# Optimization experiments

Hardware: AMD Instinct MI355X
Metric: run time of the kernel (lower is better)

The kernel has to match this reference:

```python
import jax, jax.numpy as jnp
import numpy as np

EMBED_DIM = 1024
NUM_HEADS = 16
HEAD_DIM = EMBED_DIM // NUM_HEADS
TGT_LEN = 1024
SRC_LEN = 1024
BSZ = 4


def setup_inputs() -> dict:
    key = jax.random.key(0)
    ks = jax.random.split(key, 7)
    query = jax.random.normal(ks[0], (TGT_LEN, BSZ, EMBED_DIM), dtype=jnp.float32)
    key_t = jax.random.normal(ks[1], (SRC_LEN, BSZ, EMBED_DIM), dtype=jnp.float32)
    # hard 0/1 multiplicative mask applied post-softmax
    hard_attention = jax.random.randint(ks[2], (BSZ, TGT_LEN, SRC_LEN), 0, 2).astype(jnp.float32)
    # xavier_uniform_ on [3E, E]
    limit = float(np.sqrt(6.0 / (3 * EMBED_DIM + EMBED_DIM)))
    in_proj_weight = jax.random.uniform(ks[3], (3 * EMBED_DIM, EMBED_DIM), dtype=jnp.float32,
                                        minval=-limit, maxval=limit)
    in_proj_bias = jnp.zeros((3 * EMBED_DIM,), dtype=jnp.float32)
    limit_o = float(np.sqrt(1.0 / EMBED_DIM))
    out_proj_weight = jax.random.uniform(ks[4], (EMBED_DIM, EMBED_DIM), dtype=jnp.float32,
                                         minval=-limit_o, maxval=limit_o)
    out_proj_bias = jnp.zeros((EMBED_DIM,), dtype=jnp.float32)
    return {
        "query": query,
        "key": key_t,
        "hard_attention": hard_attention,
        "in_proj_weight": in_proj_weight,
        "in_proj_bias": in_proj_bias,
        "out_proj_weight": out_proj_weight,
        "out_proj_bias": out_proj_bias,
    }


def reference(query, key, hard_attention, in_proj_weight, in_proj_bias,
              out_proj_weight, out_proj_bias):
    tgt_len, bsz, embed_dim = query.shape
    src_len = key.shape[0]
    h, hd = NUM_HEADS, embed_dim // NUM_HEADS
    scaling = float(hd) ** -0.5

    # QKV projections (F.linear uses y = x @ W.T + b)
    wq = in_proj_weight[:embed_dim]
    wkv = in_proj_weight[embed_dim:]
    bq = in_proj_bias[:embed_dim]
    bkv = in_proj_bias[embed_dim:]
    q = jnp.einsum('tbe,fe->tbf', query, wq) + bq          # [T,B,E]
    kv = jnp.einsum('sbe,fe->sbf', key, wkv) + bkv          # [S,B,2E]
    k, v = jnp.split(kv, 2, axis=-1)

    q = (q * scaling).reshape(tgt_len, bsz, h, hd).transpose(1, 2, 0, 3)  # [B,H,T,D]
    k = k.reshape(src_len, bsz, h, hd).transpose(1, 2, 0, 3)              # [B,H,S,D]
    v = v.reshape(src_len, bsz, h, hd).transpose(1, 2, 0, 3)              # [B,H,S,D]

    scores = jnp.einsum('bhtd,bhsd->bhts', q, k)            # [B,H,T,S]
    attn = jax.nn.softmax(scores, axis=-1)
    # dropout_p = 0.0 -> identity
    attn = attn * hard_attention[:, None, :, :]             # post-softmax hard mask

    out = jnp.einsum('bhts,bhsd->bhtd', attn, v)            # [B,H,T,D]
    out = out.transpose(2, 0, 1, 3).reshape(tgt_len, bsz, embed_dim)
    out = jnp.einsum('tbe,fe->tbf', out, out_proj_weight) + out_proj_bias

    avg_weights = attn.sum(axis=1) / h                      # [B,T,S]
    return (out, avg_weights)
```

## Files before the change

kernel.cpp:

```cpp
#include <hip/hip_runtime.h>
#include <cstdint>
#include <cstddef>

typedef __bf16 bf16x8 __attribute__((ext_vector_type(8)));
typedef float  f32x4  __attribute__((ext_vector_type(4)));
typedef unsigned short u16x8 __attribute__((ext_vector_type(8)));

__device__ __forceinline__ uint16_t f2bf(float f) {
  uint32_t u = __float_as_uint(f);
  u += 0x7fffu + ((u >> 16) & 1u);
  return (uint16_t)(u >> 16);
}
__device__ __forceinline__ float bf2f(uint16_t u) {
  return __uint_as_float((uint32_t)u << 16);
}
__device__ __forceinline__ uint32_t cvtpk(float lo, float hi) {
  uint32_t r;
  asm("v_cvt_pk_bf16_f32 %0, %1, %2" : "=v"(r) : "v"(lo), "v"(hi));
  return r;
}

__device__ __forceinline__ f32x4 mfma16(bf16x8 a, bf16x8 b, f32x4 c) {
  return __builtin_amdgcn_mfma_f32_16x16x32_bf16(a, b, c, 0, 0, 0);
}

#define GLD_TO_LDS16(gptr, lptr)                                                   \
  __builtin_amdgcn_global_load_lds(                                                \
      (const __attribute__((address_space(1))) void*)(gptr),                       \
      (__attribute__((address_space(3))) void*)(lptr), 16, 0, 0)

__global__ void prep(const float* __restrict__ q, const float* __restrict__ k,
                     const float* __restrict__ w, const float* __restrict__ wo,
                     const float* __restrict__ hard,
                     uint16_t* __restrict__ Xq, uint16_t* __restrict__ Xk,
                     uint16_t* __restrict__ Wb, uint16_t* __restrict__ Wob,
                     uint32_t* __restrict__ bits) {
  const int bid = blockIdx.x;
  if (bid < 12288) {
    int i = bid * 256 + threadIdx.x;
    const float* src;
    uint16_t* dst;
    int off;
    if (i < 1048576)      { src = q;  dst = Xq;  off = i; }
    else if (i < 2097152) { src = k;  dst = Xk;  off = i - 1048576; }
    else if (i < 2883584) { src = w;  dst = Wb;  off = i - 2097152; }
    else                  { src = wo; dst = Wob; off = i - 2883584; }
    float4 v = ((const float4*)src)[off];
    ushort4 o;
    o.x = f2bf(v.x); o.y = f2bf(v.y); o.z = f2bf(v.z); o.w = f2bf(v.w);
    ((ushort4*)dst)[off] = o;
  } else {
    int base = (bid - 12288) * 1024;
#pragma unroll
    for (int c = 0; c < 4; c++) {
      int i = base + c * 256 + threadIdx.x;
      unsigned long long m = __ballot(hard[i] != 0.0f);
      if ((threadIdx.x & 63) == 0) {
        int wd = i >> 5;
        bits[wd]     = (uint32_t)m;
        bits[wd + 1] = (uint32_t)(m >> 32);
      }
    }
  }
}

__global__ __launch_bounds__(256)
void gemm_qkv(const uint16_t* __restrict__ Xq, const uint16_t* __restrict__ Xk,
              const uint16_t* __restrict__ Wb, const float* __restrict__ ipb,
              uint16_t* __restrict__ Qb, uint16_t* __restrict__ Kb,
              uint16_t* __restrict__ Vt) {
  __shared__ __align__(16) char As[128 * 128];
  __shared__ __align__(16) char Bs[128 * 128];
  const int tid  = threadIdx.x;
  const int wave = tid >> 6, lane = tid & 63;
  const int quad = lane >> 4, l16 = lane & 15;
  const int sw = (l16 & 7) << 4;

  const int swz = (blockIdx.x & 7) * 96 + (blockIdx.x >> 3);
  const uint16_t *A, *B;
  const float* bias;
  int bm, bn, mode;
  if (swz < 256) {
    mode = 0; A = Xq; B = Wb; bias = ipb;
    bm = swz >> 3; bn = swz & 7;
  } else {
    mode = 1; A = Xk; B = Wb + (1 << 20); bias = ipb + 1024;
    int t = swz - 256; bm = t >> 4; bn = t & 15;
  }
  const int wm = (wave >> 1) << 6, wn = (wave & 1) << 6;

  const int lrow = lane >> 3;
  const int scol = ((lane & 7) ^ lrow) << 4;
  const char* Ag = (const char*)A + (size_t)(bm * 128) * 2048;
  const char* Bg = (const char*)B + (size_t)(bn * 128) * 2048;

  f32x4 acc[4][4] = {};

  for (int k0 = 0; k0 < 2048; k0 += 128) {
    __syncthreads();
#pragma unroll
    for (int j = 0; j < 4; j++) {
      const int rbase = j * 32 + wave * 8;
      GLD_TO_LDS16(Ag + (size_t)(rbase + lrow) * 2048 + k0 + scol,
                   As + rbase * 128);
      GLD_TO_LDS16(Bg + (size_t)(rbase + lrow) * 2048 + k0 + scol,
                   Bs + rbase * 128);
    }
    __syncthreads();

    bf16x8 af[4][2], bfr[4][2];
#pragma unroll
    for (int i = 0; i < 4; i++) {
      const char* pa = As + (wm + i * 16 + l16) * 128;
      const char* pb = Bs + (wn + i * 16 + l16) * 128;
#pragma unroll
      for (int ks = 0; ks < 2; ks++) {
        af[i][ks]  = *(const bf16x8*)(pa + ((ks * 64 + quad * 16) ^ sw));
        bfr[i][ks] = *(const bf16x8*)(pb + ((ks * 64 + quad * 16) ^ sw));
      }
    }
#pragma unroll
    for (int ks = 0; ks < 2; ks++)
#pragma unroll
      for (int mi = 0; mi < 4; mi++)
#pragma unroll
        for (int ni = 0; ni < 4; ni++)
          acc[mi][ni] = mfma16(af[mi][ks], bfr[ni][ks], acc[mi][ni]);
  }

#pragma unroll
  for (int mi = 0; mi < 4; mi++)
#pragma unroll
    for (int ni = 0; ni < 4; ni++)
#pragma unroll
      for (int r = 0; r < 4; r++) {
        int gi = bm * 128 + wm + mi * 16 + quad * 4 + r;
        int gf = bn * 128 + wn + ni * 16 + l16;
        float c = acc[mi][ni][r] + bias[gf];
        if (mode == 0) {
          c *= 0.125f;
          int t = gi >> 2, b = gi & 3, h = gf >> 6, d = gf & 63;
          Qb[((((size_t)b * 16 + h) * 1024 + t) << 6) + d] = f2bf(c);
        } else {
          int s = gi >> 2, b = gi & 3;
          if (gf < 1024) {
            int h = gf >> 6, d = gf & 63;
            Kb[((((size_t)b * 16 + h) * 1024 + s) << 6) + d] = f2bf(c);
          } else {
            int fv = gf - 1024, h = fv >> 6, d = fv & 63;
            Vt[((((size_t)b * 16 + h) * 64 + d) << 10) + s] = f2bf(c);
          }
        }
      }
}

__global__ __launch_bounds__(256, 2)
void attn_kernel(const uint16_t* __restrict__ qb, const uint16_t* __restrict__ kb,
                 const uint16_t* __restrict__ vtb, const uint32_t* __restrict__ bits,
                 uint16_t* __restrict__ attn_out, float* __restrict__ rlout) {
  __shared__ __align__(16) uint16_t Ks[128 * 64];
  __shared__ __align__(16) uint16_t Vs[64 * 128];
  __shared__ __align__(16) uint16_t Pb[4 * 32 * 128];

  const int bid = blockIdx.x;
  const int xcd = bid & 7, j = bid >> 3;
  const int slab = xcd * 8 + (j >> 3);
  const int b = slab >> 4, h = slab & 15;
  const int t0 = (j & 7) << 7;
  const int tid = threadIdx.x, wave = tid >> 6, lane = tid & 63;
  const int quad = lane >> 4, l16 = lane & 15;
  const int sw = (l16 & 7) << 4;
  const size_t bh = (size_t)b * 16 + h;
  const int tw = t0 + wave * 32;
  const int ta = tw + l16, tb = ta + 16;
  char* PwA = (char*)(Pb + wave * (32 * 128)) + l16 * 256;
  char* PwB = PwA + 16 * 256;

  const uint16_t* qA = qb + ((bh << 10) + ta) * 64;
  bf16x8 aqA0 = *(const bf16x8*)(qA + quad * 8);
  bf16x8 aqA1 = *(const bf16x8*)(qA + 32 + quad * 8);
  bf16x8 aqB0 = *(const bf16x8*)(qA + 1024 + quad * 8);
  bf16x8 aqB1 = *(const bf16x8*)(qA + 1024 + 32 + quad * 8);

  f32x4 accA[4] = {}, accB[4] = {};
  float smA = 0.f, smB = 0.f;

  const int kr = tid >> 3, kc8 = tid & 7;
  const int vr = tid >> 4, vc16 = tid & 15;

  const uint32_t* bA = bits + (((size_t)(b << 10) + ta) << 5);
  const uint32_t* bB = bits + (((size_t)(b << 10) + tb) << 5);

  u16x8 kreg[4], vreg[4];
#pragma unroll
  for (int r = 0; r < 4; r++)
    kreg[r] = *(const u16x8*)(kb + (bh << 16) + (size_t)(r * 256 + tid) * 8);
#pragma unroll
  for (int r = 0; r < 4; r++)
    vreg[r] = *(const u16x8*)(vtb + (((bh << 6) + r * 16 + vr) << 10) + vc16 * 8);
  uint4 uA = *(const uint4*)bA;
  uint4 uB = *(const uint4*)bB;

  for (int sc = 0; sc < 8; sc++) {
    uint32_t wA[4] = {uA.x >> (quad * 4), uA.y >> (quad * 4),
                      uA.z >> (quad * 4), uA.w >> (quad * 4)};
    uint32_t wB[4] = {uB.x >> (quad * 4), uB.y >> (quad * 4),
                      uB.z >> (quad * 4), uB.w >> (quad * 4)};

    __syncthreads();
#pragma unroll
    for (int r = 0; r < 4; r++) {
      const int row = r * 32 + kr;
      *(u16x8*)((char*)Ks + row * 128 + ((kc8 * 16) ^ ((row & 7) << 4))) = kreg[r];
    }
#pragma unroll
    for (int r = 0; r < 4; r++) {
      const int row = r * 16 + vr;
      *(u16x8*)((char*)Vs + row * 256 + ((vc16 * 16) ^ ((row & 7) << 4))) = vreg[r];
    }
    __syncthreads();

    if (sc < 7) {
      const uint16_t* kbase = kb + (bh << 16) + (size_t)(sc + 1) * 8192;
#pragma unroll
      for (int r = 0; r < 4; r++)
        kreg[r] = *(const u16x8*)(kbase + (size_t)(r * 256 + tid) * 8);
#pragma unroll
      for (int r = 0; r < 4; r++)
        vreg[r] = *(const u16x8*)(vtb + (((bh << 6) + r * 16 + vr) << 10) +
                                  (sc + 1) * 128 + vc16 * 8);
      uA = *(const uint4*)(bA + (sc + 1) * 4);
      uB = *(const uint4*)(bB + (sc + 1) * 4);
    }

#pragma unroll
    for (int nn = 0; nn < 8; nn++) {
      const char* kbp = (const char*)Ks + (nn * 16 + l16) * 128;
      bf16x8 bk0 = *(const bf16x8*)(kbp + ((quad * 16) ^ sw));
      bf16x8 bk1 = *(const bf16x8*)(kbp + ((64 + quad * 16) ^ sw));
      f32x4 cA = {}, cB = {};
      cA = mfma16(bk0, aqA0, cA); cA = mfma16(bk1, aqA1, cA);
      cB = mfma16(bk0, aqB0, cB); cB = mfma16(bk1, aqB1, cB);
      const uint32_t mA = wA[nn >> 1] >> ((nn & 1) * 16);
      const uint32_t mB = wB[nn >> 1] >> ((nn & 1) * 16);
      float eA[4], eB[4];
#pragma unroll
      for (int r = 0; r < 4; r++) {
        eA[r] = __expf(cA[r]); smA += eA[r];
        eB[r] = __expf(cB[r]); smB += eB[r];
        eA[r] = ((mA >> r) & 1) ? eA[r] : 0.f;
        eB[r] = ((mB >> r) & 1) ? eB[r] : 0.f;
      }
      const int pc = (nn * 32 + quad * 8) ^ sw;
      *(uint2*)(PwA + pc) = make_uint2(cvtpk(eA[0], eA[1]), cvtpk(eA[2], eA[3]));
      *(uint2*)(PwB + pc) = make_uint2(cvtpk(eB[0], eB[1]), cvtpk(eB[2], eB[3]));
    }

#pragma unroll
    for (int kc = 0; kc < 4; kc++) {
      const int pcb = (kc * 64 + quad * 16) ^ sw;
      bf16x8 apA = *(const bf16x8*)(PwA + pcb);
      bf16x8 apB = *(const bf16x8*)(PwB + pcb);
#pragma unroll
      for (int dt = 0; dt < 4; dt++) {
        bf16x8 bv = *(const bf16x8*)((const char*)Vs + (dt * 16 + l16) * 256 +
                                     ((kc * 64 + quad * 16) ^ sw));
        accA[dt] = mfma16(bv, apA, accA[dt]);
        accB[dt] = mfma16(bv, apB, accB[dt]);
      }
    }
  }

  smA += __shfl_xor(smA, 16); smA += __shfl_xor(smA, 32);
  smB += __shfl_xor(smB, 16); smB += __shfl_xor(smB, 32);
  const float rlA = 1.0f / smA, rlB = 1.0f / smB;
  if (quad == 0) rlout[(bh << 10) + ta] = rlA;
  if (quad == 1) rlout[(bh << 10) + tb] = rlB;

#pragma unroll
  for (int dt = 0; dt < 4; dt++) {
    uint2 oA = make_uint2(cvtpk(accA[dt][0] * rlA, accA[dt][1] * rlA),
                          cvtpk(accA[dt][2] * rlA, accA[dt][3] * rlA));
    *(uint2*)(attn_out + ((size_t)(ta * 4 + b) << 10) + h * 64 + dt * 16 + quad * 4) = oA;
    uint2 oB = make_uint2(cvtpk(accB[dt][0] * rlB, accB[dt][1] * rlB),
                          cvtpk(accB[dt][2] * rlB, accB[dt][3] * rlB));
    *(uint2*)(attn_out + ((size_t)(tb * 4 + b) << 10) + h * 64 + dt * 16 + quad * 4) = oB;
  }
}

__global__ __launch_bounds__(256, 4)
void tail(const uint16_t* __restrict__ qb, const uint16_t* __restrict__ kb,
          const float* __restrict__ rlin, const float* __restrict__ hard,
          const uint16_t* __restrict__ Ao, const uint16_t* __restrict__ Bw,
          const float* __restrict__ opb,
          float* __restrict__ out, float* __restrict__ avgout) {
  __shared__ __align__(16) char smem[24576];
  const int bid = blockIdx.x;
  const int tid = threadIdx.x, wave = tid >> 6, lane = tid & 63;
  const int quad = lane >> 4, l16 = lane & 15;

  if (bid < 512) {
    uint16_t* Ks = (uint16_t*)smem;
    const int xcd = bid & 7, j = bid >> 3;
    const int slab = xcd * 4 + (j >> 4);
    const int b  = slab >> 3;
    const int s0 = (slab & 7) << 7;
    const int t0 = (j & 15) << 6;
    const int sw = (l16 & 7) << 4;
    const int tr = t0 + wave * 16 + l16;
    const int kr = tid >> 3, kc8 = tid & 7;

    float av[8][4] = {};

    u16x8 kreg[4];
    {
      const uint16_t* kb0 = kb + ((((size_t)b * 16) << 10) + s0) * 64;
#pragma unroll
      for (int r = 0; r < 4; r++)
        kreg[r] = *(const u16x8*)(kb0 + (size_t)(r * 256 + tid) * 8);
    }

    for (int hh = 0; hh < 16; hh++) {
      __syncthreads();
#pragma unroll
      for (int r = 0; r < 4; r++) {
        const int row = r * 32 + kr;
        *(u16x8*)((char*)Ks + row * 128 + ((kc8 * 16) ^ ((row & 7) << 4))) = kreg[r];
      }
      __syncthreads();
      if (hh < 15) {
        const uint16_t* kb2 = kb + ((((size_t)b * 16 + hh + 1) << 10) + s0) * 64;
#pragma unroll
        for (int r = 0; r < 4; r++)
          kreg[r] = *(const u16x8*)(kb2 + (size_t)(r * 256 + tid) * 8);
      }

      const size_t bh = (size_t)b * 16 + hh;
      const uint16_t* qrow = qb + ((bh << 10) + tr) * 64;
      bf16x8 aq0 = *(const bf16x8*)(qrow + quad * 8);
      bf16x8 aq1 = *(const bf16x8*)(qrow + 32 + quad * 8);
      const float rl = rlin[(bh << 10) + tr];

#pragma unroll
      for (int n = 0; n < 8; n++) {
        const char* kbp = (const char*)Ks + (n * 16 + l16) * 128;
        bf16x8 bk0 = *(const bf16x8*)(kbp + ((quad * 16) ^ sw));
        bf16x8 bk1 = *(const bf16x8*)(kbp + ((64 + quad * 16) ^ sw));
        f32x4 c = {};
        c = mfma16(bk0, aq0, c);
        c = mfma16(bk1, aq1, c);
#pragma unroll
        for (int r = 0; r < 4; r++) av[n][r] += __expf(c[r]) * rl;
      }
    }

    const float* hrow = hard + (((size_t)(b << 10) + tr) << 10) + s0 + quad * 4;
    float* orow = avgout + ((size_t)(b << 10) + tr) * 1024 + s0 + quad * 4;
#pragma unroll
    for (int n = 0; n < 8; n++) {
      float4 hm = *(const float4*)(hrow + n * 16);
      float4 f;
      f.x = av[n][0] * (hm.x != 0.f ? 0.0625f : 0.f);
      f.y = av[n][1] * (hm.y != 0.f ? 0.0625f : 0.f);
      f.z = av[n][2] * (hm.z != 0.f ? 0.0625f : 0.f);
      f.w = av[n][3] * (hm.w != 0.f ? 0.0625f : 0.f);
      *(float4*)(orow + n * 16) = f;
    }
  } else {
    char* As = smem;
    char* Bs = smem + 8192;
    const int u = bid - 512;
    const int swz = (u & 7) * 64 + (u >> 3);
    const int bm = swz >> 3, bn = swz & 7;
    const int wm = (wave >> 1) << 5, wn = (wave & 1) << 6;
    const int sw = (l16 & 7) << 4;
    const int lrow = lane >> 3;
    const int scol = ((lane & 7) ^ lrow) << 4;
    const char* Ag = (const char*)Ao + (size_t)(bm * 64) * 2048;
    const char* Bg = (const char*)Bw + (size_t)(bn * 128) * 2048;

    f32x4 acc[2][4] = {};

    for (int k0 = 0; k0 < 2048; k0 += 128) {
      __syncthreads();
#pragma unroll
      for (int jj = 0; jj < 2; jj++) {
        const int rbase = jj * 32 + wave * 8;
        GLD_TO_LDS16(Ag + (size_t)(rbase + lrow) * 2048 + k0 + scol,
                     As + rbase * 128);
      }
#pragma unroll
      for (int jj = 0; jj < 4; jj++) {
        const int rbase = jj * 32 + wave * 8;
        GLD_TO_LDS16(Bg + (size_t)(rbase + lrow) * 2048 + k0 + scol,
                     Bs + rbase * 128);
      }
      __syncthreads();

      bf16x8 af[2][2], bfr[4][2];
#pragma unroll
      for (int i = 0; i < 2; i++) {
        const char* pa = As + (wm + i * 16 + l16) * 128;
#pragma unroll
        for (int ks = 0; ks < 2; ks++)
          af[i][ks] = *(const bf16x8*)(pa + ((ks * 64 + quad * 16) ^ sw));
      }
#pragma unroll
      for (int i = 0; i < 4; i++) {
        const char* pb = Bs + (wn + i * 16 + l16) * 128;
#pragma unroll
        for (int ks = 0; ks < 2; ks++)
          bfr[i][ks] = *(const bf16x8*)(pb + ((ks * 64 + quad * 16) ^ sw));
      }
#pragma unroll
      for (int ks = 0; ks < 2; ks++)
#pragma unroll
        for (int mi = 0; mi < 2; mi++)
#pragma unroll
          for (int ni = 0; ni < 4; ni++)
            acc[mi][ni] = mfma16(af[mi][ks], bfr[ni][ks], acc[mi][ni]);
    }

#pragma unroll
    for (int mi = 0; mi < 2; mi++)
#pragma unroll
      for (int ni = 0; ni < 4; ni++)
#pragma unroll
        for (int r = 0; r < 4; r++) {
          int gi = bm * 64 + wm + mi * 16 + quad * 4 + r;
          int gf = bn * 128 + wn + ni * 16 + l16;
          out[(size_t)gi * 1024 + gf] = acc[mi][ni][r] + opb[gf];
        }
  }
}

extern "C" void kernel_launch(void* const* d_in, const int* in_sizes, int n_in,
                              void* d_out, int out_size, void* d_ws, size_t ws_size,
                              hipStream_t stream) {
  const float* query = (const float*)d_in[0];
  const float* key   = (const float*)d_in[1];
  const float* hard  = (const float*)d_in[2];
  const float* ipw   = (const float*)d_in[3];
  const float* ipb   = (const float*)d_in[4];
  const float* opw   = (const float*)d_in[5];
  const float* opb   = (const float*)d_in[6];

  char* ws = (char*)d_ws;
  const size_t MB = 1ull << 20;
  uint16_t* Xq  = (uint16_t*)(ws + 0);
  uint16_t* Xk  = (uint16_t*)(ws + 8 * MB);
  uint16_t* Wb  = (uint16_t*)(ws + 16 * MB);
  uint16_t* Wob = (uint16_t*)(ws + 22 * MB);
  uint16_t* Qb  = (uint16_t*)(ws + 24 * MB);
  uint16_t* Kb  = (uint16_t*)(ws + 32 * MB);
  uint16_t* Vt  = (uint16_t*)(ws + 40 * MB);
  uint16_t* AO  = Xq;
  float*    rlws = (float*)(ws + 8 * MB);

  float* out = (float*)d_out;
  float* avg = out + 4194304;
  uint32_t* bits = (uint32_t*)out;

  prep<<<16384, 256, 0, stream>>>(query, key, ipw, opw, hard,
                                  Xq, Xk, Wb, Wob, bits);

  gemm_qkv<<<768, 256, 0, stream>>>(Xq, Xk, Wb, ipb, Qb, Kb, Vt);

  attn_kernel<<<512, 256, 0, stream>>>(Qb, Kb, Vt, bits, AO, rlws);

  tail<<<1024, 256, 0, stream>>>(Qb, Kb, rlws, hard, AO, Wob, opb, out, avg);
}
```

Baseline: 228.8 us.

## Load V fragments directly from global and process two heads per tail iteration

The attention kernel drops the shared-memory staging of V. Each lane now loads its V^T MFMA operand fragments straight from global memory into registers, and launch bounds are raised to 3 blocks per CU. The tail kernel stages K for two heads per barrier pair, with the LDS buffer enlarged to 32KB, which halves the number of synchronisations and gives more work per pass. The risks are uncoalesced or redundant global V loads across waves, higher register pressure that could cause spilling under the tighter bound, and lower occupancy in the tail kernel from the larger LDS footprint.

```diff
diff --git a/kernel.cpp b/kernel.cpp
--- a/kernel.cpp
+++ b/kernel.cpp
@@ -154,12 +154,11 @@
       }
 }
 
-__global__ __launch_bounds__(256, 2)
+__global__ __launch_bounds__(256, 3)
 void attn_kernel(const uint16_t* __restrict__ qb, const uint16_t* __restrict__ kb,
                  const uint16_t* __restrict__ vtb, const uint32_t* __restrict__ bits,
                  uint16_t* __restrict__ attn_out, float* __restrict__ rlout) {
   __shared__ __align__(16) uint16_t Ks[128 * 64];
-  __shared__ __align__(16) uint16_t Vs[64 * 128];
   __shared__ __align__(16) uint16_t Pb[4 * 32 * 128];
 
   const int bid = blockIdx.x;
@@ -186,18 +185,16 @@
   float smA = 0.f, smB = 0.f;
 
   const int kr = tid >> 3, kc8 = tid & 7;
-  const int vr = tid >> 4, vc16 = tid & 15;
 
   const uint32_t* bA = bits + (((size_t)(b << 10) + ta) << 5);
   const uint32_t* bB = bits + (((size_t)(b << 10) + tb) << 5);
 
-  u16x8 kreg[4], vreg[4];
+  const uint16_t* vbase = vtb + ((bh << 6) + l16) * 1024 + quad * 8;
+
+  u16x8 kreg[4];
 #pragma unroll
   for (int r = 0; r < 4; r++)
     kreg[r] = *(const u16x8*)(kb + (bh << 16) + (size_t)(r * 256 + tid) * 8);
-#pragma unroll
-  for (int r = 0; r < 4; r++)
-    vreg[r] = *(const u16x8*)(vtb + (((bh << 6) + r * 16 + vr) << 10) + vc16 * 8);
   uint4 uA = *(const uint4*)bA;
   uint4 uB = *(const uint4*)bB;
 
@@ -213,22 +210,20 @@
       const int row = r * 32 + kr;
       *(u16x8*)((char*)Ks + row * 128 + ((kc8 * 16) ^ ((row & 7) << 4))) = kreg[r];
     }
-#pragma unroll
-    for (int r = 0; r < 4; r++) {
-      const int row = r * 16 + vr;
-      *(u16x8*)((char*)Vs + row * 256 + ((vc16 * 16) ^ ((row & 7) << 4))) = vreg[r];
-    }
     __syncthreads();
+
+    bf16x8 vf[4][4];
+#pragma unroll
+    for (int kc = 0; kc < 4; kc++)
+#pragma unroll
+      for (int dt = 0; dt < 4; dt++)
+        vf[kc][dt] = *(const bf16x8*)(vbase + (dt << 14) + sc * 128 + kc * 32);
 
     if (sc < 7) {
       const uint16_t* kbase = kb + (bh << 16) + (size_t)(sc + 1) * 8192;
 #pragma unroll
       for (int r = 0; r < 4; r++)
         kreg[r] = *(const u16x8*)(kbase + (size_t)(r * 256 + tid) * 8);
-#pragma unroll
-      for (int r = 0; r < 4; r++)
-        vreg[r] = *(const u16x8*)(vtb + (((bh << 6) + r * 16 + vr) << 10) +
-                                  (sc + 1) * 128 + vc16 * 8);
       uA = *(const uint4*)(bA + (sc + 1) * 4);
       uB = *(const uint4*)(bB + (sc + 1) * 4);
     }
@@ -263,10 +258,8 @@
       bf16x8 apB = *(const bf16x8*)(PwB + pcb);
 #pragma unroll
       for (int dt = 0; dt < 4; dt++) {
-        bf16x8 bv = *(const bf16x8*)((const char*)Vs + (dt * 16 + l16) * 256 +
-                                     ((kc * 64 + quad * 16) ^ sw));
-        accA[dt] = mfma16(bv, apA, accA[dt]);
-        accB[dt] = mfma16(bv, apB, accB[dt]);
+        accA[dt] = mfma16(vf[kc][dt], apA, accA[dt]);
+        accB[dt] = mfma16(vf[kc][dt], apB, accB[dt]);
       }
     }
   }
@@ -294,13 +287,12 @@
           const uint16_t* __restrict__ Ao, const uint16_t* __restrict__ Bw,
           const float* __restrict__ opb,
           float* __restrict__ out, float* __restrict__ avgout) {
-  __shared__ __align__(16) char smem[24576];
+  __shared__ __align__(16) char smem[32768];
   const int bid = blockIdx.x;
   const int tid = threadIdx.x, wave = tid >> 6, lane = tid & 63;
   const int quad = lane >> 4, l16 = lane & 15;
 
   if (bid < 512) {
-    uint16_t* Ks = (uint16_t*)smem;
     const int xcd = bid & 7, j = bid >> 3;
     const int slab = xcd * 4 + (j >> 4);
     const int b  = slab >> 3;
@@ -308,49 +300,52 @@
     const int t0 = (j & 15) << 6;
     const int sw = (l16 & 7) << 4;
     const int tr = t0 + wave * 16 + l16;
-    const int kr = tid >> 3, kc8 = tid & 7;
+    const int krow = tid >> 3, kc8 = tid & 7;
 
     float av[8][4] = {};
 
-    u16x8 kreg[4];
-    {
-      const uint16_t* kb0 = kb + ((((size_t)b * 16) << 10) + s0) * 64;
+    u16x8 krgA[4], krgB[4];
+    auto loadK = [&](int hh, u16x8* krg) {
+      const uint16_t* kb0 = kb + ((((size_t)b * 16 + hh) << 10) + s0) * 64;
 #pragma unroll
       for (int r = 0; r < 4; r++)
-        kreg[r] = *(const u16x8*)(kb0 + (size_t)(r * 256 + tid) * 8);
-    }
-
-    for (int hh = 0; hh < 16; hh++) {
+        krg[r] = *(const u16x8*)(kb0 + (size_t)(r * 256 + tid) * 8);
+    };
+    loadK(0, krgA); loadK(1, krgB);
+
+    for (int hp = 0; hp < 8; hp++) {
       __syncthreads();
 #pragma unroll
       for (int r = 0; r < 4; r++) {
-        const int row = r * 32 + kr;
-        *(u16x8*)((char*)Ks + row * 128 + ((kc8 * 16) ^ ((row & 7) << 4))) = kreg[r];
+        const int row = r * 32 + krow;
+        const int off = row * 128 + ((kc8 * 16) ^ ((row & 7) << 4));
+        *(u16x8*)(smem + off) = krgA[r];
+        *(u16x8*)(smem + 16384 + off) = krgB[r];
       }
       __syncthreads();
-      if (hh < 15) {
-        const uint16_t* kb2 = kb + ((((size_t)b * 16 + hh + 1) << 10) + s0) * 64;
-#pragma unroll
-        for (int r = 0; r < 4; r++)
-          kreg[r] = *(const u16x8*)(kb2 + (size_t)(r * 256 + tid) * 8);
-      }
-
-      const size_t bh = (size_t)b * 16 + hh;
-      const uint16_t* qrow = qb + ((bh << 10) + tr) * 64;
-      bf16x8 aq0 = *(const bf16x8*)(qrow + quad * 8);
-      bf16x8 aq1 = *(const bf16x8*)(qrow + 32 + quad * 8);
-      const float rl = rlin[(bh << 10) + tr];
-
-#pragma unroll
-      for (int n = 0; n < 8; n++) {
-        const char* kbp = (const char*)Ks + (n * 16 + l16) * 128;
-        bf16x8 bk0 = *(const bf16x8*)(kbp + ((quad * 16) ^ sw));
-        bf16x8 bk1 = *(const bf16x8*)(kbp + ((64 + quad * 16) ^ sw));
-        f32x4 c = {};
-        c = mfma16(bk0, aq0, c);
-        c = mfma16(bk1, aq1, c);
-#pragma unroll
-        for (int r = 0; r < 4; r++) av[n][r] += __expf(c[r]) * rl;
+      if (hp < 7) { loadK(hp * 2 + 2, krgA); loadK(hp * 2 + 3, krgB); }
+
+#pragma unroll
+      for (int hs = 0; hs < 2; hs++) {
+        const int hh = hp * 2 + hs;
+        const char* Kbase = smem + hs * 16384;
+        const size_t bh = (size_t)b * 16 + hh;
+        const uint16_t* qrow = qb + ((bh << 10) + tr) * 64;
+        bf16x8 aq0 = *(const bf16x8*)(qrow + quad * 8);
+        bf16x8 aq1 = *(const bf16x8*)(qrow + 32 + quad * 8);
+        const float rl = rlin[(bh << 10) + tr];
+
+#pragma unroll
+        for (int n = 0; n < 8; n++) {
+          const char* kbp = Kbase + (n * 16 + l16) * 128;
+          bf16x8 bk0 = *(const bf16x8*)(kbp + ((quad * 16) ^ sw));
+          bf16x8 bk1 = *(const bf16x8*)(kbp + ((64 + quad * 16) ^ sw));
+          f32x4 c = {};
+          c = mfma16(bk0, aq0, c);
+          c = mfma16(bk1, aq1, c);
+#pragma unroll
+          for (int r = 0; r < 4; r++) av[n][r] += __expf(c[r]) * rl;
+        }
       }
     }
 
```

Result: slower. 268.7 us (+17.5%).
